# Optimization experiments

Hardware: AMD Instinct MI355X
Metric: run time of the kernel (lower is better)

## Reference

```python
import jax, jax.numpy as jnp
import numpy as np

B, N, D_OBJ, D_Q, D_FUSED, D_BOX, D_ATT = 64, 36, 2048, 2048, 2048, 4, 512


def setup_inputs() -> dict:
    key = jax.random.key(0)
    ks = jax.random.split(key, 12)
    s = lambda d: 1.0 / np.sqrt(d)
    return {
        "question_embedding": jax.random.normal(ks[0], (B * N, D_Q), jnp.float32),
        "object_features_list": jax.random.normal(ks[1], (B, N, D_OBJ), jnp.float32),
        "bounding_boxes": jax.random.uniform(ks[2], (B, N, D_BOX), jnp.float32),
        "Wq": jax.random.normal(ks[3], (D_Q, D_FUSED), jnp.float32) * s(D_Q),
        "Wo": jax.random.normal(ks[4], (D_OBJ, D_FUSED), jnp.float32) * s(D_OBJ),
        "Wfa": jax.random.normal(ks[5], (D_FUSED, D_FUSED), jnp.float32) * s(D_FUSED),
        "Wfb": jax.random.normal(ks[6], (D_FUSED, D_FUSED), jnp.float32) * s(D_FUSED),
        "Wba": jax.random.normal(ks[7], (D_BOX, D_FUSED), jnp.float32) * s(D_BOX),
        "Wbb": jax.random.normal(ks[8], (D_BOX, D_FUSED), jnp.float32) * s(D_BOX),
        "W0": jax.random.normal(ks[9], (D_FUSED, D_ATT), jnp.float32) * s(D_FUSED),
        "b0": jnp.zeros((D_ATT,), jnp.float32),
        "W1": jax.random.normal(ks[10], (D_ATT, 1), jnp.float32) * s(D_ATT),
        "b1": jnp.zeros((1,), jnp.float32),
        "batch_size": B,
        "num_obj": N,
    }


def reference(question_embedding, object_features_list, bounding_boxes,
              Wq, Wo, Wfa, Wfb, Wba, Wbb, W0, b0, W1, b1,
              batch_size, num_obj):
    # fuse_object_features_with_questions: MLB fusion of question and objects
    obj_flat = object_features_list.reshape(batch_size * num_obj, -1)  # [BN, D]
    fused = (question_embedding @ Wq) * (obj_flat @ Wo)                # [BN, Df]
    fused = fused.reshape(batch_size, num_obj, -1)                     # [B, N, Df]

    # pairwise: project once, broadcast-multiply instead of materializing
    # expanded [B*N*N, D] operands (same math as expand+view+fusion).
    ra = fused @ Wfa                 # [B, N, Df]
    rb = fused @ Wfb                 # [B, N, Df]
    ba = bounding_boxes @ Wba        # [B, N, Df]
    bb = bounding_boxes @ Wbb        # [B, N, Df]
    # relations[b, i, j, :] = fusion_fused(f_i, f_j) + fusion_box(box_i, box_j)
    relations = ra[:, :, None, :] * rb[:, None, :, :] + ba[:, :, None, :] * bb[:, None, :, :]  # [B,N,N,Df]

    # compute_relation_attention: linear-tanh-linear, softmax over dim=2
    h = jnp.tanh(relations @ W0 + b0)          # [B, N, N, D_att]
    scores = h @ W1 + b1                       # [B, N, N, 1]
    att = jax.nn.softmax(scores, axis=2)[..., 0]  # [B, N, N]
    e_hat = jnp.sum(relations * att[..., None], axis=2)  # [B, N, Df]

    pairwise_res = fused + e_hat
    return object_features_list + pairwise_res
```

## Files before the change

### kernel.cpp

```cpp
#include <hip/hip_runtime.h>
#include <hip/hip_bf16.h>
#include <math.h>

constexpr int kB    = 64;
constexpr int kN    = 36;
constexpr int kBN   = kB * kN;
constexpr int kD    = 2048;
constexpr int kDatt = 512;
constexpr int kPairs = kN * kN;

using bf16x8 = __attribute__((ext_vector_type(8))) short;
using f32x4  = __attribute__((ext_vector_type(4))) float;

typedef unsigned int u32;
typedef __attribute__((address_space(3))) u32 lds_u32;
typedef const __attribute__((address_space(1))) u32 glb_u32;


__device__ inline unsigned short f2bf(float f) {
    union { float f; unsigned u; } v; v.f = f;
    unsigned r = v.u + 0x7FFFu + ((v.u >> 16) & 1u);
    return (unsigned short)(r >> 16);
}

__global__ __launch_bounds__(256)
void kcvt_t(const float* __restrict__ x, unsigned short* __restrict__ y)
{
    int i = blockIdx.x * 256 + threadIdx.x;
    if (i >= kBN * (kD / 4)) return;
    float4 v = ((const float4*)x)[i];
    ushort4 o = {f2bf(v.x), f2bf(v.y), f2bf(v.z), f2bf(v.w)};
    int row = i >> 9;
    int kf  = (i & 511) << 2;
    int kb = kf >> 5;
    int chunk = row >> 4, rl = row & 15;
    int g = (rl & 7) | (((kf >> 3) & 3) << 3) | ((rl >> 3) << 5);
    *(ushort4*)&y[(size_t)kb * (144 * 512) + chunk * 512 + g * 8 + (kf & 7)] = o;
}

__global__ __launch_bounds__(256)
void kzero(float* __restrict__ p, int n)
{
    int i = blockIdx.x * 256 + threadIdx.x;
    if (i < n) p[i] = 0.f;
}

__global__ __launch_bounds__(256)
void ktrp(const float* __restrict__ W, unsigned short* __restrict__ WT, int nt)
{
    __shared__ float T[64][65];
    const int k0 = blockIdx.x * 64;
    const int n0 = blockIdx.y * 64;
    const int c = threadIdx.x & 63, r0 = threadIdx.x >> 6;
    #pragma unroll
    for (int rr = 0; rr < 64; rr += 4)
        T[r0 + rr][c] = W[(size_t)(k0 + r0 + rr) * nt + n0 + c];
    __syncthreads();
    #pragma unroll
    for (int rr = 0; rr < 64; rr += 4)
        WT[(size_t)(n0 + r0 + rr) * kD + k0 + c] = f2bf(T[c][r0 + rr]);
}

__global__ __launch_bounds__(256)
void ktrp_t(const float* __restrict__ W, unsigned short* __restrict__ Wt)
{
    __shared__ float T[64][65];
    const int k0 = blockIdx.x * 64;
    const int n0 = blockIdx.y * 64;
    const int c = threadIdx.x & 63, r0 = threadIdx.x >> 6;
    #pragma unroll
    for (int rr = 0; rr < 64; rr += 4)
        T[r0 + rr][c] = W[(size_t)(k0 + r0 + rr) * kD + n0 + c];
    __syncthreads();
    #pragma unroll
    for (int rr = 0; rr < 64; rr += 4) {
        int row = n0 + r0 + rr;
        int k   = k0 + c;
        int kb = k >> 5, kl = k & 31;
        int chunk = row >> 4, rl = row & 15;
        int g = (rl & 7) | (((kl >> 3) & 3) << 3) | ((rl >> 3) << 5);
        Wt[(size_t)kb * (128 * 512) + chunk * 512 + g * 8 + (kl & 7)] = f2bf(T[c][r0 + rr]);
    }
}

__global__ __launch_bounds__(64)
void krepack_w0(const unsigned short* __restrict__ W0T, unsigned short* __restrict__ W0s)
{
    const int kb    = blockIdx.x;
    const int chunk = blockIdx.y;
    const int g     = threadIdx.x;
    const int row = chunk * 16 + (g & 7) + ((g >> 5) << 3);
    const int cg8 = ((g >> 3) & 3) * 8;
    const uint4 v = *(const uint4*)&W0T[(size_t)row * kD + kb * 32 + cg8];
    *(uint4*)&W0s[(size_t)kb * 16384 + chunk * 512 + g * 8] = v;
}

__global__ __launch_bounds__(256)
void kgbox(const float* __restrict__ Wba, const float* __restrict__ Wbb,
           const float* __restrict__ W0, float* __restrict__ Gpart)
{
    __shared__ float red[4][64][17];
    const int ct = blockIdx.x;
    const int kc = blockIdx.y;
    const int cl = threadIdx.x & 63;
    const int kq = threadIdx.x >> 6;
    const int c  = ct * 64 + cl;

    float acc[16];
    #pragma unroll
    for (int t = 0; t < 16; ++t) acc[t] = 0.f;

    const int kbase = kc * 128 + kq * 32;
    for (int kk = 0; kk < 32; ++kk) {
        int k = kbase + kk;
        float w0 = W0[(size_t)k * kDatt + c];
        float a0 = Wba[k], a1 = Wba[kD + k], a2 = Wba[2 * kD + k], a3 = Wba[3 * kD + k];
        float b0 = Wbb[k] * w0, b1 = Wbb[kD + k] * w0,
              b2 = Wbb[2 * kD + k] * w0, b3 = Wbb[3 * kD + k] * w0;
        acc[0]  = fmaf(a0, b0, acc[0]);  acc[1]  = fmaf(a0, b1, acc[1]);
        acc[2]  = fmaf(a0, b2, acc[2]);  acc[3]  = fmaf(a0, b3, acc[3]);
        acc[4]  = fmaf(a1, b0, acc[4]);  acc[5]  = fmaf(a1, b1, acc[5]);
        acc[6]  = fmaf(a1, b2, acc[6]);  acc[7]  = fmaf(a1, b3, acc[7]);
        acc[8]  = fmaf(a2, b0, acc[8]);  acc[9]  = fmaf(a2, b1, acc[9]);
        acc[10] = fmaf(a2, b2, acc[10]); acc[11] = fmaf(a2, b3, acc[11]);
        acc[12] = fmaf(a3, b0, acc[12]); acc[13] = fmaf(a3, b1, acc[13]);
        acc[14] = fmaf(a3, b2, acc[14]); acc[15] = fmaf(a3, b3, acc[15]);
    }
    #pragma unroll
    for (int t = 0; t < 16; ++t) red[kq][cl][t] = acc[t];
    __syncthreads();
    #pragma unroll
    for (int t = 0; t < 4; ++t) {
        int s = threadIdx.x + t * 256;
        int cc = s >> 4, uv = s & 15;
        float v = red[0][cc][uv] + red[1][cc][uv] + red[2][cc][uv] + red[3][cc][uv];
        Gpart[((size_t)kc * 16 + uv) * kDatt + ct * 64 + cc] = v;
    }
}

__global__ __launch_bounds__(64)
void krepack_g(const float* __restrict__ Gpart, unsigned short* __restrict__ W0s)
{
    const int chunk = blockIdx.x;
    const int g     = threadIdx.x;
    const int col = chunk * 16 + (g & 7) + ((g >> 5) << 3);
    const int kg  = (g >> 3) & 3;
    unsigned short o[8];
    #pragma unroll
    for (int e = 0; e < 8; ++e) {
        int kl = kg * 8 + e;
        if (kl < 16) {
            float s = 0.f;
            #pragma unroll
            for (int kc = 0; kc < 16; ++kc)
                s += Gpart[((size_t)kc * 16 + kl) * kDatt + col];
            o[e] = f2bf(s);
        } else o[e] = 0;
    }
    *(uint4*)&W0s[(size_t)64 * 16384 + chunk * 512 + g * 8] = *(uint4*)o;
}

__global__ __launch_bounds__(256, 2)
void k1_dual_mfma(const unsigned short* __restrict__ Qt,
                  const unsigned short* __restrict__ Wqt,
                  const unsigned short* __restrict__ Ot,
                  const unsigned short* __restrict__ Wot,
                  unsigned short* __restrict__ fusedt)
{
    __shared__ __align__(16) unsigned short As1[128 * 32];
    __shared__ __align__(16) unsigned short As2[128 * 32];
    __shared__ __align__(16) unsigned short Bs1[64 * 32];
    __shared__ __align__(16) unsigned short Bs2[64 * 32];

    const int tid = threadIdx.x;
    const int lane = tid & 63;
    const int w = tid >> 6;
    const int wm = w >> 1, wn = w & 1;
    const int row0 = blockIdx.y * 128;
    const int col0 = blockIdx.x * 64;
    const int chA = row0 >> 4;
    const int chB = col0 >> 4;

    f32x4 acc1[4][2], acc2[4][2];
    #pragma unroll
    for (int mt = 0; mt < 4; ++mt)
        #pragma unroll
        for (int nt = 0; nt < 2; ++nt) { acc1[mt][nt] = (f32x4)(0.f); acc2[mt][nt] = (f32x4)(0.f); }

    const int fr = lane & 15, fq = lane >> 4;
    const int inoff = ((fr & 7) << 3) | (fq << 6) | ((fr >> 3) << 8);

    for (int kb = 0; kb < 64; ++kb) {
        #pragma unroll
        for (int t = 0; t < 2; ++t) {
            int cl = w * 2 + t;
            __builtin_amdgcn_global_load_lds((glb_u32*)(Qt + ((size_t)kb * 144 + chA + cl) * 512 + lane * 8),
                                             (lds_u32*)&As1[cl * 512], 16, 0, 0);
            __builtin_amdgcn_global_load_lds((glb_u32*)(Ot + ((size_t)kb * 144 + chA + cl) * 512 + lane * 8),
                                             (lds_u32*)&As2[cl * 512], 16, 0, 0);
        }
        __builtin_amdgcn_global_load_lds((glb_u32*)(Wqt + ((size_t)kb * 128 + chB + w) * 512 + lane * 8),
                                         (lds_u32*)&Bs1[w * 512], 16, 0, 0);
        __builtin_amdgcn_global_load_lds((glb_u32*)(Wot + ((size_t)kb * 128 + chB + w) * 512 + lane * 8),
                                         (lds_u32*)&Bs2[w * 512], 16, 0, 0);
        __syncthreads();

        bf16x8 a1[4], a2[4];
        #pragma unroll
        for (int mt = 0; mt < 4; ++mt) {
            a1[mt] = *(bf16x8*)&As1[(wm * 4 + mt) * 512 + inoff];
            a2[mt] = *(bf16x8*)&As2[(wm * 4 + mt) * 512 + inoff];
        }
        #pragma unroll
        for (int nt = 0; nt < 2; ++nt) {
            bf16x8 b1 = *(bf16x8*)&Bs1[(wn * 2 + nt) * 512 + inoff];
            bf16x8 b2 = *(bf16x8*)&Bs2[(wn * 2 + nt) * 512 + inoff];
            #pragma unroll
            for (int mt = 0; mt < 4; ++mt) {
                acc1[mt][nt] = __builtin_amdgcn_mfma_f32_16x16x32_bf16(a1[mt], b1, acc1[mt][nt], 0, 0, 0);
                acc2[mt][nt] = __builtin_amdgcn_mfma_f32_16x16x32_bf16(a2[mt], b2, acc2[mt][nt], 0, 0, 0);
            }
        }
        __syncthreads();
    }

    #pragma unroll
    for (int mt = 0; mt < 4; ++mt)
        #pragma unroll
        for (int nt = 0; nt < 2; ++nt) {
            #pragma unroll
            for (int reg = 0; reg < 4; ++reg) {
                int row = row0 + wm * 64 + mt * 16 + fq * 4 + reg;
                int col = col0 + wn * 32 + nt * 16 + fr;
                float v = acc1[mt][nt][reg] * acc2[mt][nt][reg];
                int kbo = col >> 5, kl = col & 31;
                int chunk = row >> 4, rl = row & 15;
                int g = (rl & 7) | (((kl >> 3) & 3) << 3) | ((rl >> 3) << 5);
                fusedt[(size_t)kbo * (144 * 512) + chunk * 512 + g * 8 + (kl & 7)] = f2bf(v);
            }
        }
}

__global__ __launch_bounds__(256, 2)
void k2_dual_mfma(const unsigned short* __restrict__ Ft,
                  const unsigned short* __restrict__ Wfat,
                  const unsigned short* __restrict__ Wfbt,
                  float* __restrict__ ra, float* __restrict__ rb)
{
    __shared__ __align__(16) unsigned short As [128 * 32];
    __shared__ __align__(16) unsigned short Bs1[64 * 32];
    __shared__ __align__(16) unsigned short Bs2[64 * 32];

    const int tid = threadIdx.x;
    const int lane = tid & 63;
    const int w = tid >> 6;
    const int wm = w >> 1, wn = w & 1;
    const int row0 = blockIdx.y * 128;
    const int col0 = blockIdx.x * 64;
    const int chA = row0 >> 4;
    const int chB = col0 >> 4;

    f32x4 acc1[4][2], acc2[4][2];
    #pragma unroll
    for (int mt = 0; mt < 4; ++mt)
        #pragma unroll
        for (int nt = 0; nt < 2; ++nt) { acc1[mt][nt] = (f32x4)(0.f); acc2[mt][nt] = (f32x4)(0.f); }

    const int fr = lane & 15, fq = lane >> 4;
    const int inoff = ((fr & 7) << 3) | (fq << 6) | ((fr >> 3) << 8);

    for (int kb = 0; kb < 64; ++kb) {
        #pragma unroll
        for (int t = 0; t < 2; ++t) {
            int cl = w * 2 + t;
            __builtin_amdgcn_global_load_lds((glb_u32*)(Ft + ((size_t)kb * 144 + chA + cl) * 512 + lane * 8),
                                             (lds_u32*)&As[cl * 512], 16, 0, 0);
        }
        __builtin_amdgcn_global_load_lds((glb_u32*)(Wfat + ((size_t)kb * 128 + chB + w) * 512 + lane * 8),
                                         (lds_u32*)&Bs1[w * 512], 16, 0, 0);
        __builtin_amdgcn_global_load_lds((glb_u32*)(Wfbt + ((size_t)kb * 128 + chB + w) * 512 + lane * 8),
                                         (lds_u32*)&Bs2[w * 512], 16, 0, 0);
        __syncthreads();

        bf16x8 a[4];
        #pragma unroll
        for (int mt = 0; mt < 4; ++mt)
            a[mt] = *(bf16x8*)&As[(wm * 4 + mt) * 512 + inoff];
        #pragma unroll
        for (int nt = 0; nt < 2; ++nt) {
            bf16x8 b1 = *(bf16x8*)&Bs1[(wn * 2 + nt) * 512 + inoff];
            bf16x8 b2 = *(bf16x8*)&Bs2[(wn * 2 + nt) * 512 + inoff];
            #pragma unroll
            for (int mt = 0; mt < 4; ++mt) {
                acc1[mt][nt] = __builtin_amdgcn_mfma_f32_16x16x32_bf16(a[mt], b1, acc1[mt][nt], 0, 0, 0);
                acc2[mt][nt] = __builtin_amdgcn_mfma_f32_16x16x32_bf16(a[mt], b2, acc2[mt][nt], 0, 0, 0);
            }
        }
        __syncthreads();
    }

    #pragma unroll
    for (int mt = 0; mt < 4; ++mt)
        #pragma unroll
        for (int nt = 0; nt < 2; ++nt) {
            int row = row0 + wm * 64 + mt * 16 + fq * 4;
            int col = col0 + wn * 32 + nt * 16 + fr;
            #pragma unroll
            for (int reg = 0; reg < 4; ++reg) {
                size_t o = (size_t)(row + reg) * kD + col;
                ra[o] = acc1[mt][nt][reg];
                rb[o] = acc2[mt][nt][reg];
            }
        }
}

__global__ __launch_bounds__(512, 4)
void k4_scores_mfma(const float* __restrict__ ra, const float* __restrict__ rb,
                    const float* __restrict__ box,
                    const unsigned short* __restrict__ W0s,
                    const float* __restrict__ b0, const float* __restrict__ W1,
                    float* __restrict__ scores)
{
    __shared__ __align__(16) unsigned short Bs[2][256 * 32];
    __shared__ __align__(16) unsigned short RelS[2][128][40];
    __shared__ __align__(16) float4 Stg4[2][378];
    __shared__ float scoreS[128];

    const int tid  = threadIdx.x;
    const int lane = tid & 63;
    const int w    = tid >> 6;
    const int wm   = w >> 2;
    const int wn   = w & 3;

    const int work = (blockIdx.x & 7) * 176 + (blockIdx.x >> 3);
    const int colb = work & 1;
    const int wt   = work >> 1;
    const int b    = wt / 11;
    const int tile = wt - b * 11;
    const int p0   = tile * 128;
    const int i0   = p0 / kN;

    const float* raB  = ra  + (size_t)b * kN * kD;
    const float* rbB  = rb  + (size_t)b * kN * kD;
    const float* boxB = box + (size_t)b * kN * 4;

    const bool hasStage = (tid < 336);
    const float* sptr;
    int sdst;
    {
        int s = hasStage ? tid : 335;
        int row = s >> 3, q = s & 7;
        int grow; const float* base;
        if (row < 6) {
            int il = (row < 5) ? row : 4;
            grow = i0 + il; if (grow > kN - 1) grow = kN - 1;
            base = raB;
        } else {
            grow = row - 6;
            base = rbB;
        }
        sptr = base + (size_t)grow * kD + q * 4;
        sdst = row * 9 + q;
    }

    int rowA, cg2, iA, jA, sA, sR;
    {
        rowA = tid >> 2; cg2 = tid & 3;
        int p = p0 + rowA; if (p >= kPairs) p = kPairs - 1;
        iA = p / kN;
        jA = p - iA * kN;
        int ilA = iA - i0;
        sA = ilA * 9 + cg2 * 2;
        sR = (6 + jA) * 9 + cg2 * 2;
    }

    const int fr = lane & 15, fq = lane >> 4;
    const int bco = ((fr & 7) << 3) + ((fr >> 3) << 8) + (fq << 6);

    f32x4 acc[4][4];
    #pragma unroll
    for (int mt = 0; mt < 4; ++mt)
        #pragma unroll
        for (int nt = 0; nt < 4; ++nt)
            acc[mt][nt] = (f32x4)(0.f);

    if (tid < 128) scoreS[tid] = 0.f;

    float4 sreg0;

    #define ISSUE_B(k0_, buf_)                                                   \
        _Pragma("unroll")                                                        \
        for (int t = 0; t < 2; ++t) {                                            \
            int ch = w * 2 + t;                                                  \
            const unsigned short* gp = W0s + (size_t)((k0_) >> 5) * 16384        \
                                       + (colb * 16 + ch) * 512 + lane * 8;      \
            __builtin_amdgcn_global_load_lds((glb_u32*)gp,                       \
                (lds_u32*)&Bs[buf_][ch * 512], 16, 0, 0);                        \
        }

    #define STAGE_LOAD(k0_) {                                                    \
            if (hasStage) sreg0 = *(const float4*)(sptr + (k0_));                \
        }

    #define STAGE_WRITE(buf_) {                                                  \
            if (hasStage) Stg4[buf_][sdst] = sreg0;                              \
        }

    #define REL_GEN(buf_) {                                                      \
            float4 va0 = Stg4[buf_][sA],     va1 = Stg4[buf_][sA + 1];           \
            float4 vr0 = Stg4[buf_][sR],     vr1 = Stg4[buf_][sR + 1];           \
            unsigned short o[8];                                                 \
            o[0] = f2bf(va0.x * vr0.x); o[1] = f2bf(va0.y * vr0.y);              \
            o[2] = f2bf(va0.z * vr0.z); o[3] = f2bf(va0.w * vr0.w);              \
            o[4] = f2bf(va1.x * vr1.x); o[5] = f2bf(va1.y * vr1.y);              \
            o[6] = f2bf(va1.z * vr1.z); o[7] = f2bf(va1.w * vr1.w);              \
            *(bf16x8*)&RelS[buf_][rowA][cg2 * 8] = *(bf16x8*)o;                  \
        }

    #define REL_GEN_BOX(buf_) {                                                  \
            unsigned short o[8] = {0, 0, 0, 0, 0, 0, 0, 0};                      \
            if (cg2 < 2) {                                                       \
                float4 bj = *(const float4*)(boxB + jA * 4);                     \
                float biu0 = boxB[iA * 4 + cg2 * 2];                             \
                float biu1 = boxB[iA * 4 + cg2 * 2 + 1];                         \
                o[0] = f2bf(biu0 * bj.x); o[1] = f2bf(biu0 * bj.y);              \
                o[2] = f2bf(biu0 * bj.z); o[3] = f2bf(biu0 * bj.w);              \
                o[4] = f2bf(biu1 * bj.x); o[5] = f2bf(biu1 * bj.y);              \
                o[6] = f2bf(biu1 * bj.z); o[7] = f2bf(biu1 * bj.w);              \
            }                                                                    \
            *(bf16x8*)&RelS[buf_][rowA][cg2 * 8] = *(bf16x8*)o;                  \
        }

    STAGE_LOAD(0)
    STAGE_WRITE(0)
    STAGE_LOAD(32)
    __syncthreads();
    REL_GEN(0)
    STAGE_WRITE(1)
    ISSUE_B(0, 0)

    for (int k = 0; k <= 64; ++k) {
        const int cur = k & 1, nxt = cur ^ 1;
        __syncthreads();
        if (k < 62) STAGE_LOAD((k + 2) * 32)
        if (k < 64) ISSUE_B((k + 1) * 32, nxt)
        bf16x8 af[4];
        #pragma unroll
        for (int mt = 0; mt < 4; ++mt)
            af[mt] = *(bf16x8*)&RelS[cur][wm * 64 + mt * 16 + fr][fq * 8];
        if (k < 63) REL_GEN(nxt)
        else if (k == 63) REL_GEN_BOX(nxt)
        __builtin_amdgcn_s_setprio(1);
        #pragma unroll
        for (int nt = 0; nt < 4; ++nt) {
            bf16x8 bfv = *(bf16x8*)&Bs[cur][wn * 2048 + nt * 512 + bco];
            #pragma unroll
            for (int mt = 0; mt < 4; ++mt)
                acc[mt][nt] = __builtin_amdgcn_mfma_f32_16x16x32_bf16(af[mt], bfv, acc[mt][nt], 0, 0, 0);
        }
        __builtin_amdgcn_s_setprio(0);
        if (k < 62) STAGE_WRITE(cur)
    }

    float b0v[4], w1v[4];
    #pragma unroll
    for (int nt = 0; nt < 4; ++nt) {
        int col = colb * 256 + wn * 64 + nt * 16 + fr;
        b0v[nt] = b0[col];
        w1v[nt] = W1[col];
    }
    #pragma unroll
    for (int mt = 0; mt < 4; ++mt) {
        #pragma unroll
        for (int reg = 0; reg < 4; ++reg) {
            float p = 0.f;
            #pragma unroll
            for (int nt = 0; nt < 4; ++nt)
                p += w1v[nt] * tanhf(acc[mt][nt][reg] + b0v[nt]);
            p += __shfl_xor(p, 1, 64);
            p += __shfl_xor(p, 2, 64);
            p += __shfl_xor(p, 4, 64);
            p += __shfl_xor(p, 8, 64);
            if (fr == 0)
                atomicAdd(&scoreS[wm * 64 + mt * 16 + fq * 4 + reg], p);
        }
    }
    __syncthreads();
    if (tid < 128 && p0 + tid < kPairs)
        atomicAdd(&scores[(size_t)b * kPairs + p0 + tid], scoreS[tid]);
}

__global__ __launch_bounds__(64)
void k5_softmax(const float* __restrict__ scores, const float* __restrict__ box,
                float* __restrict__ att, float* __restrict__ abox)
{
    const int bi = blockIdx.x;
    const int b  = bi / kN;
    const int tid = threadIdx.x;
    float s = (tid < kN) ? scores[(size_t)bi * kN + tid] : -1e30f;
    float m = s;
    #pragma unroll
    for (int off = 32; off >= 1; off >>= 1)
        m = fmaxf(m, __shfl_xor(m, off, 64));
    float e = (tid < kN) ? expf(s - m) : 0.f;
    float sum = e;
    #pragma unroll
    for (int off = 32; off >= 1; off >>= 1)
        sum += __shfl_xor(sum, off, 64);
    float a = e / sum;
    if (tid < kN) att[(size_t)bi * kN + tid] = a;

    float4 bx = {0.f, 0.f, 0.f, 0.f};
    if (tid < kN) bx = *(const float4*)(box + (size_t)(b * kN + tid) * 4);
    bx.x *= a; bx.y *= a; bx.z *= a; bx.w *= a;
    #pragma unroll
    for (int off = 32; off >= 1; off >>= 1) {
        bx.x += __shfl_xor(bx.x, off, 64);
        bx.y += __shfl_xor(bx.y, off, 64);
        bx.z += __shfl_xor(bx.z, off, 64);
        bx.w += __shfl_xor(bx.w, off, 64);
    }
    if (tid == 0) *(float4*)(abox + (size_t)bi * 4) = bx;
}

__global__ __launch_bounds__(256)
void k6_output(const float* __restrict__ obj, const unsigned short* __restrict__ fusedt,
               const float* __restrict__ ra, const float* __restrict__ rb,
               const float* __restrict__ att, const float* __restrict__ box,
               const float* __restrict__ abox,
               const float* __restrict__ Wba, const float* __restrict__ Wbb,
               float* __restrict__ out)
{
    __shared__ float attS[kN];
    const int bi = (blockIdx.x & 7) * 288 + (blockIdx.x >> 3);
    const int b = bi / kN;
    const int tid = threadIdx.x;
    if (tid < kN) attS[tid] = att[(size_t)bi * kN + tid];
    __syncthreads();
    const float4 bxi = *(const float4*)(box  + (size_t)bi * 4);
    const float4 axi = *(const float4*)(abox + (size_t)bi * 4);
    const int chunk = bi >> 4, rl = bi & 15;
    for (int d = tid; d < kD; d += 256) {
        float s1 = 0.f;
        #pragma unroll 4
        for (int j = 0; j < kN; ++j)
            s1 = fmaf(attS[j], rb[(size_t)(b * kN + j) * kD + d], s1);
        float bav = bxi.x * Wba[d] + bxi.y * Wba[kD + d]
                  + bxi.z * Wba[2 * kD + d] + bxi.w * Wba[3 * kD + d];
        float s2  = axi.x * Wbb[d] + axi.y * Wbb[kD + d]
                  + axi.z * Wbb[2 * kD + d] + axi.w * Wbb[3 * kD + d];
        size_t o = (size_t)bi * kD + d;
        int kbf = d >> 5, klf = d & 31;
        int g = (rl & 7) | (((klf >> 3) & 3) << 3) | ((rl >> 3) << 5);
        float fv = __uint_as_float(
            (u32)fusedt[(size_t)kbf * (144 * 512) + chunk * 512 + g * 8 + (klf & 7)] << 16);
        out[o] = obj[o] + fv + ra[o] * s1 + bav * s2;
    }
}

extern "C" void kernel_launch(void* const* d_in, const int* in_sizes, int n_in,
                              void* d_out, int out_size, void* d_ws, size_t ws_size,
                              hipStream_t stream)
{
    const float* q   = (const float*)d_in[0];
    const float* obj = (const float*)d_in[1];
    const float* box = (const float*)d_in[2];
    const float* Wq  = (const float*)d_in[3];
    const float* Wo  = (const float*)d_in[4];
    const float* Wfa = (const float*)d_in[5];
    const float* Wfb = (const float*)d_in[6];
    const float* Wba = (const float*)d_in[7];
    const float* Wbb = (const float*)d_in[8];
    const float* W0  = (const float*)d_in[9];
    const float* b0v = (const float*)d_in[10];
    const float* W1  = (const float*)d_in[11];
    float* out = (float*)d_out;

    const size_t nBD = (size_t)kBN * kD;
    float* ws = (float*)d_ws;
    size_t off = 0;
    float* ra     = ws + off; off += nBD;
    float* rb     = ws + off; off += nBD;
    float* scores = ws + off; off += (size_t)kBN * kN;
    float* att    = ws + off; off += (size_t)kBN * kN;
    float* abox   = ws + off; off += (size_t)kBN * 4;
    float* Gpart  = ws + off; off += (size_t)16 * 16 * kDatt;

    unsigned short* us = (unsigned short*)(ws + off);
    size_t uoff = 0;
    unsigned short* W0T    = us + uoff; uoff += (size_t)kDatt * kD;
    unsigned short* W0s    = us + uoff; uoff += (size_t)65 * 16384;
    unsigned short* qt     = us + uoff; uoff += nBD;
    unsigned short* objt   = us + uoff; uoff += nBD;
    unsigned short* fusedt = us + uoff; uoff += nBD;
    unsigned short* Wqt    = us + uoff; uoff += (size_t)kD * kD;
    unsigned short* Wot    = us + uoff; uoff += (size_t)kD * kD;
    unsigned short* Wfat = qt;
    unsigned short* Wfbt = objt;

    kcvt_t<<<dim3(kBN * (kD / 4) / 256), 256, 0, stream>>>(q,   qt);
    kcvt_t<<<dim3(kBN * (kD / 4) / 256), 256, 0, stream>>>(obj, objt);
    ktrp<<<dim3(32, 8), 256, 0, stream>>>(W0, W0T, kDatt);
    krepack_w0<<<dim3(64, 32), 64, 0, stream>>>(W0T, W0s);
    kgbox<<<dim3(8, 16), 256, 0, stream>>>(Wba, Wbb, W0, Gpart);
    krepack_g<<<dim3(32), 64, 0, stream>>>(Gpart, W0s);
    kzero<<<dim3((kBN * kN + 255) / 256), 256, 0, stream>>>(scores, kBN * kN);
    ktrp_t<<<dim3(32, 32), 256, 0, stream>>>(Wq, Wqt);
    ktrp_t<<<dim3(32, 32), 256, 0, stream>>>(Wo, Wot);

    k1_dual_mfma<<<dim3(kD / 64, kBN / 128), 256, 0, stream>>>(qt, Wqt, objt, Wot, fusedt);

    ktrp_t<<<dim3(32, 32), 256, 0, stream>>>(Wfa, Wfat);
    ktrp_t<<<dim3(32, 32), 256, 0, stream>>>(Wfb, Wfbt);

    k2_dual_mfma<<<dim3(kD / 64, kBN / 128), 256, 0, stream>>>(fusedt, Wfat, Wfbt, ra, rb);

    k4_scores_mfma<<<dim3(kB * 11 * 2), 512, 0, stream>>>(ra, rb, box, W0s, b0v, W1, scores);
    k5_softmax<<<kBN, 64, 0, stream>>>(scores, box, att, abox);
    k6_output<<<kBN, 256, 0, stream>>>(obj, fusedt, ra, rb, att, box, abox, Wba, Wbb, out);
}
```

Measured before the change: 622.9 us.

## Batch weight prep into fewer launches and load W0 fragments directly from global

```diff
diff --git a/kernel.cpp b/kernel.cpp
--- a/kernel.cpp
+++ b/kernel.cpp
@@ -24,8 +24,11 @@
 }
 
 __global__ __launch_bounds__(256)
-void kcvt_t(const float* __restrict__ x, unsigned short* __restrict__ y)
-{
+void kcvt2(const float* __restrict__ q, const float* __restrict__ obj,
+           unsigned short* __restrict__ qt, unsigned short* __restrict__ objt)
+{
+    const float* x = blockIdx.y ? obj : q;
+    unsigned short* y = blockIdx.y ? objt : qt;
     int i = blockIdx.x * 256 + threadIdx.x;
     if (i >= kBN * (kD / 4)) return;
     float4 v = ((const float4*)x)[i];
@@ -46,31 +49,29 @@
 }
 
 __global__ __launch_bounds__(256)
-void ktrp(const float* __restrict__ W, unsigned short* __restrict__ WT, int nt)
-{
+void ktrp5(const float* __restrict__ Wq, const float* __restrict__ Wo,
+           const float* __restrict__ Wfa, const float* __restrict__ Wfb,
+           const float* __restrict__ W0,
+           unsigned short* __restrict__ Wqt, unsigned short* __restrict__ Wot,
+           unsigned short* __restrict__ Wfat, unsigned short* __restrict__ Wfbt,
+           unsigned short* __restrict__ W0s)
+{
+    const int z = blockIdx.z;
+    const float* W; unsigned short* Wt; int nt;
+    if      (z == 0) { W = Wq;  Wt = Wqt;  nt = kD; }
+    else if (z == 1) { W = Wo;  Wt = Wot;  nt = kD; }
+    else if (z == 2) { W = Wfa; Wt = Wfat; nt = kD; }
+    else if (z == 3) { W = Wfb; Wt = Wfbt; nt = kD; }
+    else             { W = W0;  Wt = W0s;  nt = kDatt; }
+    const int n0 = blockIdx.y * 64;
+    if (n0 >= nt) return;
+    const int nch = nt >> 4;
+    const int k0 = blockIdx.x * 64;
     __shared__ float T[64][65];
-    const int k0 = blockIdx.x * 64;
-    const int n0 = blockIdx.y * 64;
     const int c = threadIdx.x & 63, r0 = threadIdx.x >> 6;
     #pragma unroll
     for (int rr = 0; rr < 64; rr += 4)
         T[r0 + rr][c] = W[(size_t)(k0 + r0 + rr) * nt + n0 + c];
-    __syncthreads();
-    #pragma unroll
-    for (int rr = 0; rr < 64; rr += 4)
-        WT[(size_t)(n0 + r0 + rr) * kD + k0 + c] = f2bf(T[c][r0 + rr]);
-}
-
-__global__ __launch_bounds__(256)
-void ktrp_t(const float* __restrict__ W, unsigned short* __restrict__ Wt)
-{
-    __shared__ float T[64][65];
-    const int k0 = blockIdx.x * 64;
-    const int n0 = blockIdx.y * 64;
-    const int c = threadIdx.x & 63, r0 = threadIdx.x >> 6;
-    #pragma unroll
-    for (int rr = 0; rr < 64; rr += 4)
-        T[r0 + rr][c] = W[(size_t)(k0 + r0 + rr) * kD + n0 + c];
     __syncthreads();
     #pragma unroll
     for (int rr = 0; rr < 64; rr += 4) {
@@ -79,20 +80,8 @@
         int kb = k >> 5, kl = k & 31;
         int chunk = row >> 4, rl = row & 15;
         int g = (rl & 7) | (((kl >> 3) & 3) << 3) | ((rl >> 3) << 5);
-        Wt[(size_t)kb * (128 * 512) + chunk * 512 + g * 8 + (kl & 7)] = f2bf(T[c][r0 + rr]);
-    }
-}
-
-__global__ __launch_bounds__(64)
-void krepack_w0(const unsigned short* __restrict__ W0T, unsigned short* __restrict__ W0s)
-{
-    const int kb    = blockIdx.x;
-    const int chunk = blockIdx.y;
-    const int g     = threadIdx.x;
-    const int row = chunk * 16 + (g & 7) + ((g >> 5) << 3);
-    const int cg8 = ((g >> 3) & 3) * 8;
-    const uint4 v = *(const uint4*)&W0T[(size_t)row * kD + kb * 32 + cg8];
-    *(uint4*)&W0s[(size_t)kb * 16384 + chunk * 512 + g * 8] = v;
+        Wt[(size_t)kb * (nch * 512) + chunk * 512 + g * 8 + (kl & 7)] = f2bf(T[c][r0 + rr]);
+    }
 }
 
 __global__ __launch_bounds__(256)
@@ -321,7 +310,6 @@
                     const float* __restrict__ b0, const float* __restrict__ W1,
                     float* __restrict__ scores)
 {
-    __shared__ __align__(16) unsigned short Bs[2][256 * 32];
     __shared__ __align__(16) unsigned short RelS[2][128][40];
     __shared__ __align__(16) float4 Stg4[2][378];
     __shared__ float scoreS[128];
@@ -376,6 +364,7 @@
 
     const int fr = lane & 15, fq = lane >> 4;
     const int bco = ((fr & 7) << 3) + ((fr >> 3) << 8) + (fq << 6);
+    const unsigned short* w0base = W0s + (size_t)(colb * 16 + wn * 4) * 512 + bco;
 
     f32x4 acc[4][4];
     #pragma unroll
@@ -387,16 +376,6 @@
     if (tid < 128) scoreS[tid] = 0.f;
 
     float4 sreg0;
-
-    #define ISSUE_B(k0_, buf_)                                                   \
-        _Pragma("unroll")                                                        \
-        for (int t = 0; t < 2; ++t) {                                            \
-            int ch = w * 2 + t;                                                  \
-            const unsigned short* gp = W0s + (size_t)((k0_) >> 5) * 16384        \
-                                       + (colb * 16 + ch) * 512 + lane * 8;      \
-            __builtin_amdgcn_global_load_lds((glb_u32*)gp,                       \
-                (lds_u32*)&Bs[buf_][ch * 512], 16, 0, 0);                        \
-        }
 
     #define STAGE_LOAD(k0_) {                                                    \
             if (hasStage) sreg0 = *(const float4*)(sptr + (k0_));                \
@@ -437,13 +416,15 @@
     __syncthreads();
     REL_GEN(0)
     STAGE_WRITE(1)
-    ISSUE_B(0, 0)
 
     for (int k = 0; k <= 64; ++k) {
         const int cur = k & 1, nxt = cur ^ 1;
         __syncthreads();
+        bf16x8 bfv[4];
+        #pragma unroll
+        for (int nt = 0; nt < 4; ++nt)
+            bfv[nt] = *(const bf16x8*)(w0base + (size_t)k * 16384 + nt * 512);
         if (k < 62) STAGE_LOAD((k + 2) * 32)
-        if (k < 64) ISSUE_B((k + 1) * 32, nxt)
         bf16x8 af[4];
         #pragma unroll
         for (int mt = 0; mt < 4; ++mt)
@@ -452,12 +433,10 @@
         else if (k == 63) REL_GEN_BOX(nxt)
         __builtin_amdgcn_s_setprio(1);
         #pragma unroll
-        for (int nt = 0; nt < 4; ++nt) {
-            bf16x8 bfv = *(bf16x8*)&Bs[cur][wn * 2048 + nt * 512 + bco];
+        for (int nt = 0; nt < 4; ++nt)
             #pragma unroll
             for (int mt = 0; mt < 4; ++mt)
-                acc[mt][nt] = __builtin_amdgcn_mfma_f32_16x16x32_bf16(af[mt], bfv, acc[mt][nt], 0, 0, 0);
-        }
+                acc[mt][nt] = __builtin_amdgcn_mfma_f32_16x16x32_bf16(af[mt], bfv[nt], acc[mt][nt], 0, 0, 0);
         __builtin_amdgcn_s_setprio(0);
         if (k < 62) STAGE_WRITE(cur)
     }
@@ -588,31 +567,23 @@
 
     unsigned short* us = (unsigned short*)(ws + off);
     size_t uoff = 0;
-    unsigned short* W0T    = us + uoff; uoff += (size_t)kDatt * kD;
     unsigned short* W0s    = us + uoff; uoff += (size_t)65 * 16384;
     unsigned short* qt     = us + uoff; uoff += nBD;
     unsigned short* objt   = us + uoff; uoff += nBD;
     unsigned short* fusedt = us + uoff; uoff += nBD;
     unsigned short* Wqt    = us + uoff; uoff += (size_t)kD * kD;
     unsigned short* Wot    = us + uoff; uoff += (size_t)kD * kD;
-    unsigned short* Wfat = qt;
-    unsigned short* Wfbt = objt;
-
-    kcvt_t<<<dim3(kBN * (kD / 4) / 256), 256, 0, stream>>>(q,   qt);
-    kcvt_t<<<dim3(kBN * (kD / 4) / 256), 256, 0, stream>>>(obj, objt);
-    ktrp<<<dim3(32, 8), 256, 0, stream>>>(W0, W0T, kDatt);
-    krepack_w0<<<dim3(64, 32), 64, 0, stream>>>(W0T, W0s);
+    unsigned short* Wfat   = us + uoff; uoff += (size_t)kD * kD;
+    unsigned short* Wfbt   = us + uoff; uoff += (size_t)kD * kD;
+
+    kcvt2<<<dim3(kBN * (kD / 4) / 256, 2), 256, 0, stream>>>(q, obj, qt, objt);
+    ktrp5<<<dim3(32, 32, 5), 256, 0, stream>>>(Wq, Wo, Wfa, Wfb, W0,
+                                               Wqt, Wot, Wfat, Wfbt, W0s);
     kgbox<<<dim3(8, 16), 256, 0, stream>>>(Wba, Wbb, W0, Gpart);
     krepack_g<<<dim3(32), 64, 0, stream>>>(Gpart, W0s);
     kzero<<<dim3((kBN * kN + 255) / 256), 256, 0, stream>>>(scores, kBN * kN);
-    ktrp_t<<<dim3(32, 32), 256, 0, stream>>>(Wq, Wqt);
-    ktrp_t<<<dim3(32, 32), 256, 0, stream>>>(Wo, Wot);
 
     k1_dual_mfma<<<dim3(kD / 64, kBN / 128), 256, 0, stream>>>(qt, Wqt, objt, Wot, fusedt);
-
-    ktrp_t<<<dim3(32, 32), 256, 0, stream>>>(Wfa, Wfat);
-    ktrp_t<<<dim3(32, 32), 256, 0, stream>>>(Wfb, Wfbt);
-
     k2_dual_mfma<<<dim3(kD / 64, kBN / 128), 256, 0, stream>>>(fusedt, Wfat, Wfbt, ra, rb);
 
     k4_scores_mfma<<<dim3(kB * 11 * 2), 512, 0, stream>>>(ra, rb, box, W0s, b0v, W1, scores);
```

Result: no change. 613.4 us (-1.5%).
